# Performance work log

Hardware: AMD Instinct MI355X
Metric: run time of the kernel (lower is better)

The kernel has to match this reference:

```python
import jax, jax.numpy as jnp
import numpy as np

B, P, S, Y_DIM, G_DIM = 4, 64, 8, 16, 48


def setup_inputs() -> dict:
    key = jax.random.key(0)
    k1, k2, k3, k4, k5, k6 = jax.random.split(key, 6)
    y = jax.random.normal(k1, (B, P, S, Y_DIM), dtype=jnp.float32)
    pairwise_g = jax.random.normal(k2, (B, P, P, S, S, G_DIM), dtype=jnp.float32)
    # k_y = Linear(2*y_dim, 1), k_g = Linear(g_dim, 1)
    Wy = jax.random.normal(k3, (2 * Y_DIM, 1), dtype=jnp.float32) / np.sqrt(2 * Y_DIM)
    by = jax.random.normal(k4, (1,), dtype=jnp.float32) * 0.01
    Wg = jax.random.normal(k5, (G_DIM, 1), dtype=jnp.float32) / np.sqrt(G_DIM)
    bg = jax.random.normal(k6, (1,), dtype=jnp.float32) * 0.01
    return {"y": y, "pairwise_g": pairwise_g, "Wy": Wy, "by": by, "Wg": Wg, "bg": bg}


def reference(y, pairwise_g, Wy, by, Wg, bg):
    # Original: y_1 = y[:,None,:,None,:,:] expanded, y_2 = y[:,:,None,:,None,:] expanded,
    # k = Linear([y_1, y_2]) + Linear(pairwise_g).
    # Linearity lets us split Wy and apply each half to the small, unexpanded y,
    # then broadcast-add -- exact same math, no (B,P,P,S,S,2*y_dim) intermediate.
    y_dim = y.shape[-1]
    ky1 = y @ Wy[:y_dim]            # (B, P, S, 1) -- contribution of y_1
    ky2 = y @ Wy[y_dim:]            # (B, P, S, 1) -- contribution of y_2
    kg = pairwise_g @ Wg + bg       # (B, P, P, S, S, 1)
    k = (kg
         + ky1[:, None, :, None, :, :]   # broadcast over dims 1 (p1) and 3 (s1)
         + ky2[:, :, None, :, None, :]   # broadcast over dims 2 (p2) and 4 (s2)
         + by)
    return k
```

## Files before the change

### kernel.cpp

```cpp
#include <hip/hip_runtime.h>


#define NBPS 2048
#define NOUT 1048576

__global__ __launch_bounds__(256) void precompute_kernel(
    const float* __restrict__ y,
    const float* __restrict__ Wy,
    const float* __restrict__ by,
    const float* __restrict__ bg,
    float* __restrict__ a,
    float* __restrict__ c) {
    int i = blockIdx.x * 256 + threadIdx.x;
    if (i >= NBPS) return;
    const float4* yv = reinterpret_cast<const float4*>(y + i * 16);
    const float4* w1 = reinterpret_cast<const float4*>(Wy);
    const float4* w2 = reinterpret_cast<const float4*>(Wy + 16);
    float sa = 0.f, sc = 0.f;
#pragma unroll
    for (int j = 0; j < 4; ++j) {
        float4 v = yv[j];
        float4 u1 = w1[j];
        float4 u2 = w2[j];
        sa += v.x * u1.x + v.y * u1.y + v.z * u1.z + v.w * u1.w;
        sc += v.x * u2.x + v.y * u2.y + v.z * u2.z + v.w * u2.w;
    }
    a[i] = sa + by[0] + bg[0];
    c[i] = sc;
}

__global__ __launch_bounds__(256) void main_kernel(
    const float* __restrict__ g,
    const float* __restrict__ Wg,
    const float* __restrict__ a,
    const float* __restrict__ c,
    float* __restrict__ out) {
    int tid = blockIdx.x * 256 + threadIdx.x;
    int o = tid >> 2;
    int t = tid & 3;

    const float4* gv = reinterpret_cast<const float4*>(g + (size_t)o * 48 + t * 12);
    const float4* wv = reinterpret_cast<const float4*>(Wg + t * 12);

    float s = 0.f;
#pragma unroll
    for (int j = 0; j < 3; ++j) {
        float4 v = gv[j];
        float4 w = wv[j];
        s += v.x * w.x + v.y * w.y + v.z * w.z + v.w * w.w;
    }
    s += __shfl_xor(s, 1);
    s += __shfl_xor(s, 2);

    if (t == 0) {
        int s2 = o & 7;
        int s1 = (o >> 3) & 7;
        int p2 = (o >> 6) & 63;
        int p1 = (o >> 12) & 63;
        int b  = o >> 18;
        float av = a[((b << 6) + p2) * 8 + s2];
        float cv = c[((b << 6) + p1) * 8 + s1];
        out[o] = s + av + cv;
    }
}

extern "C" void kernel_launch(void* const* d_in, const int* in_sizes, int n_in,
                              void* d_out, int out_size, void* d_ws, size_t ws_size,
                              hipStream_t stream) {
    const float* y  = (const float*)d_in[0];
    const float* g  = (const float*)d_in[1];
    const float* Wy = (const float*)d_in[2];
    const float* by = (const float*)d_in[3];
    const float* Wg = (const float*)d_in[4];
    const float* bg = (const float*)d_in[5];
    float* out = (float*)d_out;

    float* a = (float*)d_ws;
    float* c = a + NBPS;

    precompute_kernel<<<(NBPS + 255) / 256, 256, 0, stream>>>(y, Wy, by, bg, a, c);

    int blocks = (4 * NOUT) / 256;
    main_kernel<<<blocks, 256, 0, stream>>>(g, Wg, a, c, out);
}
```

Before: 280.5 us.

## Fuse y projection into main kernel with per-block shared-memory terms

Removes the separate precompute launch and the workspace arrays. Each block, which covers one (b,p1,p2) tile of 64 outputs, now computes its 16 y-projection terms into shared memory, followed by a __syncthreads. The g load is also re-indexed so the four lanes of an output read interleaved float4s, which makes adjacent lanes access contiguous memory and improves coalescing. The cost is redundant y dot products in every block plus a block barrier before the main work.

```diff
diff --git a/kernel.cpp b/kernel.cpp
--- a/kernel.cpp
+++ b/kernel.cpp
@@ -1,66 +1,62 @@
 #include <hip/hip_runtime.h>
 
 
-#define NBPS 2048
 #define NOUT 1048576
 
-__global__ __launch_bounds__(256) void precompute_kernel(
+__global__ __launch_bounds__(256) void fused_kernel(
+    const float* __restrict__ g,
+    const float* __restrict__ Wg,
     const float* __restrict__ y,
     const float* __restrict__ Wy,
     const float* __restrict__ by,
     const float* __restrict__ bg,
-    float* __restrict__ a,
-    float* __restrict__ c) {
-    int i = blockIdx.x * 256 + threadIdx.x;
-    if (i >= NBPS) return;
-    const float4* yv = reinterpret_cast<const float4*>(y + i * 16);
-    const float4* w1 = reinterpret_cast<const float4*>(Wy);
-    const float4* w2 = reinterpret_cast<const float4*>(Wy + 16);
-    float sa = 0.f, sc = 0.f;
+    float* __restrict__ out) {
+    __shared__ float ac[16];
+
+    int blk = blockIdx.x;
+    int tid = threadIdx.x;
+    int p2 = blk & 63;
+    int p1 = (blk >> 6) & 63;
+    int b  = blk >> 12;
+
+    if (tid < 16) {
+        int s = tid & 7;
+        int row = (tid < 8) ? (((b << 6) + p2) << 3) + s
+                            : (((b << 6) + p1) << 3) + s;
+        const float4* yv = reinterpret_cast<const float4*>(y + row * 16);
+        const float4* wv = reinterpret_cast<const float4*>(Wy + ((tid < 8) ? 0 : 16));
+        float acc = 0.f;
 #pragma unroll
-    for (int j = 0; j < 4; ++j) {
-        float4 v = yv[j];
-        float4 u1 = w1[j];
-        float4 u2 = w2[j];
-        sa += v.x * u1.x + v.y * u1.y + v.z * u1.z + v.w * u1.w;
-        sc += v.x * u2.x + v.y * u2.y + v.z * u2.z + v.w * u2.w;
+        for (int j = 0; j < 4; ++j) {
+            float4 v = yv[j];
+            float4 w = wv[j];
+            acc += v.x * w.x + v.y * w.y + v.z * w.z + v.w * w.w;
+        }
+        ac[tid] = acc + ((tid < 8) ? (by[0] + bg[0]) : 0.f);
     }
-    a[i] = sa + by[0] + bg[0];
-    c[i] = sc;
-}
+    __syncthreads();
 
-__global__ __launch_bounds__(256) void main_kernel(
-    const float* __restrict__ g,
-    const float* __restrict__ Wg,
-    const float* __restrict__ a,
-    const float* __restrict__ c,
-    float* __restrict__ out) {
-    int tid = blockIdx.x * 256 + threadIdx.x;
-    int o = tid >> 2;
+    int o_local = tid >> 2;
     int t = tid & 3;
+    size_t o = (size_t)blk * 64 + o_local;
 
-    const float4* gv = reinterpret_cast<const float4*>(g + (size_t)o * 48 + t * 12);
-    const float4* wv = reinterpret_cast<const float4*>(Wg + t * 12);
+    const float4* gv = reinterpret_cast<const float4*>(g + o * 48);
+    const float4* wv = reinterpret_cast<const float4*>(Wg);
 
     float s = 0.f;
 #pragma unroll
     for (int j = 0; j < 3; ++j) {
-        float4 v = gv[j];
-        float4 w = wv[j];
+        float4 v = gv[t + 4 * j];
+        float4 w = wv[t + 4 * j];
         s += v.x * w.x + v.y * w.y + v.z * w.z + v.w * w.w;
     }
     s += __shfl_xor(s, 1);
     s += __shfl_xor(s, 2);
 
     if (t == 0) {
-        int s2 = o & 7;
-        int s1 = (o >> 3) & 7;
-        int p2 = (o >> 6) & 63;
-        int p1 = (o >> 12) & 63;
-        int b  = o >> 18;
-        float av = a[((b << 6) + p2) * 8 + s2];
-        float cv = c[((b << 6) + p1) * 8 + s1];
-        out[o] = s + av + cv;
+        int s2 = o_local & 7;
+        int s1 = o_local >> 3;
+        out[o] = s + ac[s2] + ac[8 + s1];
     }
 }
 
@@ -75,11 +71,5 @@
     const float* bg = (const float*)d_in[5];
     float* out = (float*)d_out;
 
-    float* a = (float*)d_ws;
-    float* c = a + NBPS;
-
-    precompute_kernel<<<(NBPS + 255) / 256, 256, 0, stream>>>(y, Wy, by, bg, a, c);
-
-    int blocks = (4 * NOUT) / 256;
-    main_kernel<<<blocks, 256, 0, stream>>>(g, Wg, a, c, out);
+    fused_kernel<<<NOUT / 64, 256, 0, stream>>>(g, Wg, y, Wy, by, bg, out);
 }
```

Result: no change. 276.8 us (-1.3%).
